# Performance work log

Hardware: AMD Instinct MI355X
Metric: run time of the kernel (lower is better)

## Reference

```python
import jax, jax.numpy as jnp
import numpy as np

B, C, H, W = 8, 128, 64, 64
NL = 3           # number of hidden variables (levels)
NC = C // 2      # channels per DAT block (q_c1 == kv_c1 == 64)
NH = 4           # heads
HC = NC // NH    # head channels = 16
KS = 4           # offset conv ksize == stride (pad=0 since ksize==stride)
EPS = 1e-5


def _norm_grid(ys, xs, Hk, Wk):
    g = jnp.stack(jnp.meshgrid(ys, xs, indexing='ij'), axis=-1)  # [Hk,Wk,2] (y,x)
    g = g.at[..., 0].set(g[..., 0] / (Hk - 1.0) * 2.0 - 1.0)
    g = g.at[..., 1].set(g[..., 1] / (Wk - 1.0) * 2.0 - 1.0)
    return g


def ref_points(Hk, Wk):
    return _norm_grid(jnp.linspace(0.5, Hk - 0.5, Hk), jnp.linspace(0.5, Wk - 0.5, Wk), Hk, Wk)


def q_grid(Hq, Wq):
    return _norm_grid(jnp.arange(Hq, dtype=jnp.float32), jnp.arange(Wq, dtype=jnp.float32), Hq, Wq)


def grid_sample(img, grid):
    # torch F.grid_sample: bilinear, align_corners=True, padding_mode='zeros'
    # img [B,C,H,W]; grid [B,*spatial,2] with (x,y) in [-1,1]
    Bi, Ci, Hi, Wi = img.shape
    sp = grid.shape[1:-1]
    g = grid.reshape(Bi, -1, 2)
    x = (g[..., 0] + 1.0) * 0.5 * (Wi - 1)
    y = (g[..., 1] + 1.0) * 0.5 * (Hi - 1)
    x0 = jnp.floor(x)
    y0 = jnp.floor(y)
    wx = x - x0
    wy = y - y0

    def gather(yi, xi):
        valid = ((yi >= 0) & (yi <= Hi - 1) & (xi >= 0) & (xi <= Wi - 1)).astype(img.dtype)
        yc = jnp.clip(yi, 0, Hi - 1).astype(jnp.int32)
        xc = jnp.clip(xi, 0, Wi - 1).astype(jnp.int32)
        vals = jax.vmap(lambda im, yy, xx: im[:, yy, xx])(img, yc, xc)  # [B,C,N]
        return vals * valid[:, None, :]

    out = (gather(y0, x0) * ((1 - wy) * (1 - wx))[:, None]
           + gather(y0, x0 + 1) * ((1 - wy) * wx)[:, None]
           + gather(y0 + 1, x0) * (wy * (1 - wx))[:, None]
           + gather(y0 + 1, x0 + 1) * (wy * wx)[:, None])
    return out.reshape((Bi, Ci) + sp)


def conv1x1(x, w, b=None):
    y = jnp.einsum('oc,bchw->bohw', w, x)
    return y if b is None else y + b[None, :, None, None]


def dat_block(q_in, kv_in, p):
    # DAttentionBaseline: n_groups=1, offset_range_factor=-1, use_pe=True,
    # dwc_pe=False, no_off=False, fixed_pe=False, log_cpb=False
    (pq_w, pq_b, dw_w, dw_b, ln_g, ln_b, pw_w,
     pk_w, pk_b, pv_w, pv_b, po_w, po_b, rpe) = p
    Bq, Cq, Hq, Wq = q_in.shape
    q = conv1x1(q_in, pq_w, pq_b)                              # [B,NC,H,W]
    # offset head: depthwise conv k4 s4 pad0 -> LayerNorm(channels) -> GELU -> 1x1 -> 2ch
    off = jax.lax.conv_general_dilated(
        q, dw_w, window_strides=(KS, KS), padding='VALID',
        dimension_numbers=('NCHW', 'OIHW', 'NCHW'),
        feature_group_count=NC) + dw_b[None, :, None, None]
    mu = off.mean(axis=1, keepdims=True)
    var = off.var(axis=1, keepdims=True)
    off = (off - mu) * jax.lax.rsqrt(var + EPS) * ln_g[None, :, None, None] + ln_b[None, :, None, None]
    off = jax.nn.gelu(off, approximate=False)
    offset = jnp.einsum('oc,bchw->bhwo', pw_w, off)            # [B,Hk,Wk,2] (y,x)
    Hk, Wk = offset.shape[1:3]
    Ns = Hk * Wk
    # offset_range_factor < 0 -> no tanh scaling, clamp(offset+ref, -1, 1)
    pos = jnp.clip(offset + ref_points(Hk, Wk)[None], -1.0, 1.0)
    xs = grid_sample(kv_in, pos[..., ::-1])                    # [B,Ckv,Hk,Wk]; grid as (x,y)
    xs = xs.reshape(Bq, kv_in.shape[1], Ns)
    k = jnp.einsum('oc,bcn->bon', pk_w, xs) + pk_b[None, :, None]
    v = jnp.einsum('oc,bcn->bon', pv_w, xs) + pv_b[None, :, None]
    qh = q.reshape(Bq, NH, HC, Hq * Wq)
    kh = k.reshape(Bq, NH, HC, Ns)
    vh = v.reshape(Bq, NH, HC, Ns)
    attn = jnp.einsum('bhcm,bhcn->bhmn', qh, kh) * (HC ** -0.5)
    # relative position bias: bilinear sample of rpe table at 0.5*(q_grid - pos)
    disp = (q_grid(Hq, Wq).reshape(1, Hq * Wq, 1, 2)
            - pos.reshape(Bq, 1, Ns, 2)) * 0.5                 # [B,HW,Ns,2] (y,x)
    bias = grid_sample(jnp.broadcast_to(rpe[None], (Bq,) + rpe.shape),
                       disp[..., ::-1])                        # [B,NH,HW,Ns]
    attn = jax.nn.softmax(attn + bias, axis=-1)
    out = jnp.einsum('bhmn,bhcn->bhcm', attn, vh).reshape(Bq, NC, Hq, Wq)
    return conv1x1(out, po_w, po_b)


def setup_inputs():
    key = jax.random.key(0)
    ks = jax.random.split(key, 16)
    s = 0.1
    NB = NL * (NL - 1) // 2
    return {
        'x0': jax.random.normal(ks[0], (B, C, H, W), jnp.float32),
        'x1': jax.random.normal(ks[1], (B, C, H, W), jnp.float32),
        'x2': jax.random.normal(ks[2], (B, C, H, W), jnp.float32),
        'pq_w': jax.random.normal(ks[3], (NB, NC, NC), jnp.float32) * s,
        'pq_b': jax.random.normal(ks[4], (NB, NC), jnp.float32) * s,
        'dw_w': jax.random.normal(ks[5], (NB, NC, 1, KS, KS), jnp.float32) * s,
        'dw_b': jax.random.normal(ks[6], (NB, NC), jnp.float32) * s,
        'ln_g': jnp.ones((NB, NC), jnp.float32),
        'ln_b': jnp.zeros((NB, NC), jnp.float32),
        'pw_w': jax.random.normal(ks[7], (NB, 2, NC), jnp.float32) * s,
        'pk_w': jax.random.normal(ks[8], (NB, NC, NC), jnp.float32) * s,
        'pk_b': jax.random.normal(ks[9], (NB, NC), jnp.float32) * s,
        'pv_w': jax.random.normal(ks[10], (NB, NC, NC), jnp.float32) * s,
        'pv_b': jax.random.normal(ks[11], (NB, NC), jnp.float32) * s,
        'po_w': jax.random.normal(ks[12], (NB, NC, NC), jnp.float32) * s,
        'po_b': jax.random.normal(ks[13], (NB, NC), jnp.float32) * s,
        'rpe': jax.random.normal(ks[14], (NB, NH, 2 * H - 1, 2 * W - 1), jnp.float32) * s,
    }


def reference(x0, x1, x2, pq_w, pq_b, dw_w, dw_b, ln_g, ln_b, pw_w,
              pk_w, pk_b, pv_w, pv_b, po_w, po_b, rpe):
    hidden = [x0, x1, x2]
    results = []
    num = 0
    for i in range(NL):
        res = hidden[i]
        for j in range(i):
            p = (pq_w[num], pq_b[num], dw_w[num], dw_b[num], ln_g[num], ln_b[num],
                 pw_w[num], pk_w[num], pk_b[num], pv_w[num], pv_b[num],
                 po_w[num], po_b[num], rpe[num])
            # rev=False, use_all_channels=False: q = hidden[i][:, :C//2], kv = hidden[j][:, :C//2]
            attn = dat_block(hidden[i][:, :NC], hidden[j][:, :NC], p)
            # res -= -attn with attn placed in the LAST q_c1 channels (zeros cat on first q_c2)
            res = jnp.concatenate([res[:, :C - NC], res[:, C - NC:] + attn], axis=1)
            num += 1
        results.append(res)
    return jnp.stack(results)  # [NL,B,C,H,W]
```

## Files before the change

### kernel.cpp

```cpp
#include <hip/hip_runtime.h>
#include <math.h>


typedef _Float16 f16x4 __attribute__((ext_vector_type(4)));
typedef float f32x4 __attribute__((ext_vector_type(4)));

__global__ __launch_bounds__(256) void k_copy(
    const float* __restrict__ x0, const float* __restrict__ x1,
    const float* __restrict__ x2, float* __restrict__ out) {
  int i = blockIdx.x * 256 + threadIdx.x;
  int lvl = i >> 20;
  int idx = i & 1048575;
  const float4* src = (lvl == 0) ? (const float4*)x0
                    : (lvl == 1) ? (const float4*)x1 : (const float4*)x2;
  ((float4*)out)[i] = src[idx];
}

__global__ __launch_bounds__(256) void k_qconv(
    const float* __restrict__ x1, const float* __restrict__ x2,
    const float* __restrict__ pq_w, const float* __restrict__ pq_b,
    float* __restrict__ q_buf) {
  int wg = blockIdx.x;
  int tile = wg & 15;
  int b = (wg >> 4) & 7;
  int og = (wg >> 7) & 7;
  int num = wg >> 10;
  const float* xin = (num == 0) ? x1 : x2;
  int px = tile * 256 + threadIdx.x;
  const float* xbase = xin + b * 524288 + px;
  const float* w = pq_w + num * 4096 + og * 512;
  float acc[8];
#pragma unroll
  for (int o = 0; o < 8; ++o) acc[o] = 0.f;
#pragma unroll 8
  for (int c = 0; c < 64; ++c) {
    float xv = xbase[c * 4096];
#pragma unroll
    for (int o = 0; o < 8; ++o) acc[o] += w[o * 64 + c] * xv;
  }
  float* qb = q_buf + ((num * 8 + b) * 64 + og * 8) * 4096 + px;
  const float* bias = pq_b + num * 64 + og * 8;
#pragma unroll
  for (int o = 0; o < 8; ++o) qb[o * 4096] = acc[o] + bias[o];
}

__global__ __launch_bounds__(256) void k_offset(
    const float* __restrict__ q_buf, const float* __restrict__ dw_w,
    const float* __restrict__ dw_b, const float* __restrict__ ln_g,
    const float* __restrict__ ln_b, const float* __restrict__ pw_w,
    float* __restrict__ pos_buf) {
  int wg = blockIdx.x;
  int num = wg >> 3;
  int n = threadIdx.x;
  int oy = n >> 4, ox = n & 15;
  const float* qb = q_buf + wg * 64 * 4096;
  float off[64];
  float sum = 0.f, sumsq = 0.f;
#pragma unroll
  for (int c = 0; c < 64; ++c) {
    const float* wp = dw_w + (num * 64 + c) * 16;
    const float* qp = qb + c * 4096 + oy * 256 + ox * 4;
    float4 r0 = *(const float4*)(qp);
    float4 r1 = *(const float4*)(qp + 64);
    float4 r2 = *(const float4*)(qp + 128);
    float4 r3 = *(const float4*)(qp + 192);
    float s = dw_b[num * 64 + c];
    s += wp[0] * r0.x + wp[1] * r0.y + wp[2] * r0.z + wp[3] * r0.w;
    s += wp[4] * r1.x + wp[5] * r1.y + wp[6] * r1.z + wp[7] * r1.w;
    s += wp[8] * r2.x + wp[9] * r2.y + wp[10] * r2.z + wp[11] * r2.w;
    s += wp[12] * r3.x + wp[13] * r3.y + wp[14] * r3.z + wp[15] * r3.w;
    off[c] = s;
    sum += s;
    sumsq += s * s;
  }
  float mu = sum * 0.015625f;
  float var = sumsq * 0.015625f - mu * mu;
  float rstd = rsqrtf(var + 1e-5f);
  float offy = 0.f, offx = 0.f;
#pragma unroll
  for (int c = 0; c < 64; ++c) {
    float g = (off[c] - mu) * rstd * ln_g[num * 64 + c] + ln_b[num * 64 + c];
    g = 0.5f * g * (1.f + erff(g * 0.70710678118654752f));
    offy += pw_w[num * 128 + c] * g;
    offx += pw_w[num * 128 + 64 + c] * g;
  }
  float ref_y = (0.5f + (float)oy) * (2.f / 15.f) - 1.f;
  float ref_x = (0.5f + (float)ox) * (2.f / 15.f) - 1.f;
  float py = fminf(fmaxf(offy + ref_y, -1.f), 1.f);
  float px = fminf(fmaxf(offx + ref_x, -1.f), 1.f);
  pos_buf[(wg * 256 + n) * 2 + 0] = py;
  pos_buf[(wg * 256 + n) * 2 + 1] = px;
}

__global__ __launch_bounds__(256) void k_sample(
    const float* __restrict__ x0, const float* __restrict__ x1,
    const float* __restrict__ pos_buf, float* __restrict__ xs_buf) {
  int wg = blockIdx.x;
  int cg = wg & 7;
  int b = (wg >> 3) & 7;
  int num = wg >> 6;
  const float* xj = (num == 2) ? x1 : x0;
  int n = threadIdx.x;
  int nb = num * 8 + b;
  float py = pos_buf[(nb * 256 + n) * 2 + 0];
  float px = pos_buf[(nb * 256 + n) * 2 + 1];
  float fy = (py + 1.f) * 31.5f;
  float fx = (px + 1.f) * 31.5f;
  float y0f = floorf(fy), x0f = floorf(fx);
  float wy = fy - y0f, wx = fx - x0f;
  int y0 = (int)y0f, xi0 = (int)x0f;
  int y1 = min(y0 + 1, 63), xi1 = min(xi0 + 1, 63);
  float w00 = (1.f - wy) * (1.f - wx), w01 = (1.f - wy) * wx;
  float w10 = wy * (1.f - wx), w11 = wy * wx;
  const float* xb = xj + b * 524288;
#pragma unroll
  for (int cc = 0; cc < 8; ++cc) {
    int c = cg * 8 + cc;
    const float* p = xb + c * 4096;
    float v = w00 * p[y0 * 64 + xi0] + w01 * p[y0 * 64 + xi1] +
              w10 * p[y1 * 64 + xi0] + w11 * p[y1 * 64 + xi1];
    xs_buf[(nb * 64 + c) * 256 + n] = v;
  }
}

__global__ __launch_bounds__(256) void k_kv(
    const float* __restrict__ xs_buf, const float* __restrict__ pk_w,
    const float* __restrict__ pk_b, const float* __restrict__ pv_w,
    const float* __restrict__ pv_b, _Float16* __restrict__ k16,
    _Float16* __restrict__ v16) {
  int wg = blockIdx.x;
  int which = wg & 1;
  int rest = wg >> 1;
  int nb = rest % 24;
  int og = rest / 24;
  int num = nb >> 3;
  const float* w = (which ? pv_w : pk_w) + num * 4096 + og * 512;
  const float* bias = (which ? pv_b : pk_b) + num * 64 + og * 8;
  _Float16* ob = (which ? v16 : k16) + (nb * 64 + og * 8) * 256;
  const float* xsb = xs_buf + nb * 64 * 256;
  int n = threadIdx.x;
  float acc[8];
#pragma unroll
  for (int o = 0; o < 8; ++o) acc[o] = 0.f;
#pragma unroll 8
  for (int c = 0; c < 64; ++c) {
    float xv = xsb[c * 256 + n];
#pragma unroll
    for (int o = 0; o < 8; ++o) acc[o] += w[o * 64 + c] * xv;
  }
#pragma unroll
  for (int o = 0; o < 8; ++o) ob[o * 256 + n] = (_Float16)(acc[o] + bias[o]);
}

__global__ __launch_bounds__(128) void k_padrpe(
    const float* __restrict__ rpe, float* __restrict__ tpad) {
  int wg = blockIdx.x;
  int tbl = wg >> 7;
  int r = wg & 127;
  int c = threadIdx.x;
  int rs = min(r, 126), cs = min(c, 126);
  tpad[tbl * 16384 + r * 128 + c] = rpe[tbl * 16129 + rs * 127 + cs];
}

__global__ __launch_bounds__(256) void k_attn(
    float* __restrict__ q_buf, const _Float16* __restrict__ k16,
    const _Float16* __restrict__ v16, const float* __restrict__ pos_buf,
    const float* __restrict__ tpad) {
  int wg = blockIdx.x;
  int mblock = wg & 15;
  int h = (wg >> 4) & 3;
  int b = (wg >> 6) & 7;
  int num = wg >> 9;
  int nb = num * 8 + b;
  int tid = threadIdx.x;
  int lane = tid & 63;
  int wave = __builtin_amdgcn_readfirstlane(tid >> 6);
  int l15 = lane & 15;
  int quad = lane >> 4;

  __shared__ __align__(16) float s_T[68 * 128];
  __shared__ float4 s_wt[256];
  __shared__ int s_off[256];

  {
    const float4* Ts = (const float4*)(tpad + (num * 4 + h) * 16384 + mblock * 512);
    float4* Td = (float4*)s_T;
#pragma unroll
    for (int i = 0; i < 8; ++i) Td[tid + i * 256] = Ts[tid + i * 256];
    if (tid < 128) Td[tid + 2048] = Ts[tid + 2048];
  }

  {
    float py = pos_buf[(nb * 256 + tid) * 2 + 0];
    float px = pos_buf[(nb * 256 + tid) * 2 + 1];
    float by = 31.5f * (1.f - py);
    float bx = 31.5f * (1.f - px);
    float iyf = floorf(by), ixf = floorf(bx);
    float wy = by - iyf, wx = bx - ixf;
    float uy = 1.f - wy, ux = 1.f - wx;
    s_off[tid] = (int)iyf * 128 + (int)ixf;
    s_wt[tid] = make_float4(uy * ux, uy * wx, wy * ux, wy * wx);
  }
  __syncthreads();

  int hc = nb * 64 + h * 16;
  const _Float16* kb = k16 + hc * 256;
  const _Float16* vb = v16 + hc * 256;
  float* qb = q_buf + hc * 4096;
  const float* Trow = s_T + wave * 128 + l15;

  f16x4 qf[4];
  f32x4 O[4];
  float L[4];
#pragma unroll
  for (int mt = 0; mt < 4; ++mt) {
    int m = mblock * 256 + wave * 64 + mt * 16 + l15;
#pragma unroll
    for (int j = 0; j < 4; ++j)
      qf[mt][j] = (_Float16)qb[(quad * 4 + j) * 4096 + m];
    O[mt][0] = 0.f; O[mt][1] = 0.f; O[mt][2] = 0.f; O[mt][3] = 0.f;
    L[mt] = 0.f;
  }

#pragma unroll 2
  for (int t = 0; t < 16; ++t) {
    f16x4 kf;
#pragma unroll
    for (int j = 0; j < 4; ++j)
      kf[j] = kb[(quad * 4 + j) * 256 + t * 16 + l15];
    f16x4 vf = *(const f16x4*)(vb + l15 * 256 + t * 16 + quad * 4);

    f32x4 S[4];
#pragma unroll
    for (int mt = 0; mt < 4; ++mt) {
      f32x4 Z = {0.f, 0.f, 0.f, 0.f};
      S[mt] = __builtin_amdgcn_mfma_f32_16x16x16f16(kf, qf[mt], Z, 0, 0, 0);
    }

    f16x4 pf[4];
#pragma unroll
    for (int r = 0; r < 4; ++r) {
      int off = s_off[t * 16 + quad * 4 + r];
      float4 wt = s_wt[t * 16 + quad * 4 + r];
#pragma unroll
      for (int mt = 0; mt < 4; ++mt) {
        const float* p = Trow + mt * 16 + off;
        float bias = wt.x * p[0] + wt.y * p[1] + wt.z * p[128] + wt.w * p[129];
        float s = fmaf(S[mt][r], 0.25f, bias);
        float e = __expf(s);
        L[mt] += e;
        pf[mt][r] = (_Float16)e;
      }
    }
#pragma unroll
    for (int mt = 0; mt < 4; ++mt)
      O[mt] = __builtin_amdgcn_mfma_f32_16x16x16f16(vf, pf[mt], O[mt], 0, 0, 0);
  }

#pragma unroll
  for (int mt = 0; mt < 4; ++mt) {
    float Lm = L[mt];
    Lm += __shfl_xor(Lm, 16);
    Lm += __shfl_xor(Lm, 32);
    float rinv = 1.f / Lm;
    int m = mblock * 256 + wave * 64 + mt * 16 + l15;
#pragma unroll
    for (int r = 0; r < 4; ++r)
      qb[(quad * 4 + r) * 4096 + m] = O[mt][r] * rinv;
  }
}

__global__ __launch_bounds__(256) void k_po(
    const float* __restrict__ attn_buf, const float* __restrict__ po_w,
    const float* __restrict__ po_b, float* __restrict__ out) {
  int wg = blockIdx.x;
  int tile = wg & 15;
  int b = (wg >> 4) & 7;
  int og = (wg >> 7) & 7;
  int l = (wg >> 10) + 1;
  int px = tile * 256 + threadIdx.x;
  int nlo = (l == 1) ? 0 : 1;
  int nPasses = (l == 1) ? 1 : 2;

  float acc[8];
#pragma unroll
  for (int o = 0; o < 8; ++o) acc[o] = 0.f;

  for (int s = 0; s < nPasses; ++s) {
    int num = nlo + s;
    const float* abase = attn_buf + (num * 8 + b) * 64 * 4096 + px;
    const float* w = po_w + num * 4096 + og * 512;
#pragma unroll 8
    for (int c = 0; c < 64; ++c) {
      float xv = abase[c * 4096];
#pragma unroll
      for (int o = 0; o < 8; ++o) acc[o] += w[o * 64 + c] * xv;
    }
  }

  float* ob = out + ((l * 8 + b) * 128 + 64 + og * 8) * 4096 + px;
#pragma unroll
  for (int o = 0; o < 8; ++o) {
    float bias = po_b[nlo * 64 + og * 8 + o];
    if (l == 2) bias += po_b[128 + og * 8 + o];
    ob[o * 4096] += acc[o] + bias;
  }
}

extern "C" void kernel_launch(void* const* d_in, const int* in_sizes, int n_in,
                              void* d_out, int out_size, void* d_ws,
                              size_t ws_size, hipStream_t stream) {
  const float* x0 = (const float*)d_in[0];
  const float* x1 = (const float*)d_in[1];
  const float* x2 = (const float*)d_in[2];
  const float* pq_w = (const float*)d_in[3];
  const float* pq_b = (const float*)d_in[4];
  const float* dw_w = (const float*)d_in[5];
  const float* dw_b = (const float*)d_in[6];
  const float* ln_g = (const float*)d_in[7];
  const float* ln_b = (const float*)d_in[8];
  const float* pw_w = (const float*)d_in[9];
  const float* pk_w = (const float*)d_in[10];
  const float* pk_b = (const float*)d_in[11];
  const float* pv_w = (const float*)d_in[12];
  const float* pv_b = (const float*)d_in[13];
  const float* po_w = (const float*)d_in[14];
  const float* po_b = (const float*)d_in[15];
  const float* rpe = (const float*)d_in[16];
  float* out = (float*)d_out;
  float* ws = (float*)d_ws;

  float* q_buf = ws;
  float* pos_buf = q_buf + 6291456;
  float* xs_buf = pos_buf + 12288;
  float* k_buf = xs_buf + 393216;
  float* v_buf = k_buf + 393216;
  float* tpad = xs_buf;
  _Float16* k16 = (_Float16*)k_buf;
  _Float16* v16 = (_Float16*)v_buf;

  hipLaunchKernelGGL(k_copy, dim3(12288), dim3(256), 0, stream, x0, x1, x2, out);
  hipLaunchKernelGGL(k_qconv, dim3(3072), dim3(256), 0, stream, x1, x2, pq_w,
                     pq_b, q_buf);
  hipLaunchKernelGGL(k_offset, dim3(24), dim3(256), 0, stream, q_buf, dw_w,
                     dw_b, ln_g, ln_b, pw_w, pos_buf);
  hipLaunchKernelGGL(k_sample, dim3(192), dim3(256), 0, stream, x0, x1,
                     pos_buf, xs_buf);
  hipLaunchKernelGGL(k_kv, dim3(384), dim3(256), 0, stream, xs_buf, pk_w, pk_b,
                     pv_w, pv_b, k16, v16);
  hipLaunchKernelGGL(k_padrpe, dim3(1536), dim3(128), 0, stream, rpe, tpad);
  hipLaunchKernelGGL(k_attn, dim3(1536), dim3(256), 0, stream, q_buf, k16,
                     v16, pos_buf, tpad);
  hipLaunchKernelGGL(k_po, dim3(2048), dim3(256), 0, stream, q_buf, po_w, po_b,
                     out);
}
```

Measured before the change: 281.3 us.

## Parallelize offset and sample kernels; store RPE table as fp16 and use exp2

k_offset now splits each pixel's 64 channels across 4 thread groups and combines the partial LayerNorm and projection sums with wave shuffles, launching 96 blocks instead of 24. k_sample handles 4 channels per block instead of 8, doubling the grid. In k_attn the shared-memory relative-position table is stored as fp16, halving LDS footprint and traffic. The softmax folds log2(e) into the bilinear weights and the score scale so it can call the hardware exp2 directly. The fp16 bias table lowers precision of the position bias, and the extra shuffles add a little overhead to the offset kernel.

```diff
diff --git a/kernel.cpp b/kernel.cpp
--- a/kernel.cpp
+++ b/kernel.cpp
@@ -50,14 +50,21 @@
     const float* __restrict__ ln_b, const float* __restrict__ pw_w,
     float* __restrict__ pos_buf) {
   int wg = blockIdx.x;
-  int num = wg >> 3;
-  int n = threadIdx.x;
+  int ptile = wg & 3;
+  int nb = wg >> 2;
+  int num = nb >> 3;
+  int tid = threadIdx.x;
+  int pix_lo = tid & 15;
+  int cg = (tid >> 4) & 3;
+  int pix_hi = tid >> 6;
+  int n = ptile * 64 + pix_hi * 16 + pix_lo;
   int oy = n >> 4, ox = n & 15;
-  const float* qb = q_buf + wg * 64 * 4096;
-  float off[64];
+  const float* qb = q_buf + nb * 64 * 4096;
+  float off_r[16];
   float sum = 0.f, sumsq = 0.f;
 #pragma unroll
-  for (int c = 0; c < 64; ++c) {
+  for (int cc = 0; cc < 16; ++cc) {
+    int c = cg * 16 + cc;
     const float* wp = dw_w + (num * 64 + c) * 16;
     const float* qp = qb + c * 4096 + oy * 256 + ox * 4;
     float4 r0 = *(const float4*)(qp);
@@ -69,36 +76,43 @@
     s += wp[4] * r1.x + wp[5] * r1.y + wp[6] * r1.z + wp[7] * r1.w;
     s += wp[8] * r2.x + wp[9] * r2.y + wp[10] * r2.z + wp[11] * r2.w;
     s += wp[12] * r3.x + wp[13] * r3.y + wp[14] * r3.z + wp[15] * r3.w;
-    off[c] = s;
+    off_r[cc] = s;
     sum += s;
     sumsq += s * s;
   }
+  sum += __shfl_xor(sum, 16);   sum += __shfl_xor(sum, 32);
+  sumsq += __shfl_xor(sumsq, 16); sumsq += __shfl_xor(sumsq, 32);
   float mu = sum * 0.015625f;
   float var = sumsq * 0.015625f - mu * mu;
   float rstd = rsqrtf(var + 1e-5f);
   float offy = 0.f, offx = 0.f;
 #pragma unroll
-  for (int c = 0; c < 64; ++c) {
-    float g = (off[c] - mu) * rstd * ln_g[num * 64 + c] + ln_b[num * 64 + c];
+  for (int cc = 0; cc < 16; ++cc) {
+    int c = cg * 16 + cc;
+    float g = (off_r[cc] - mu) * rstd * ln_g[num * 64 + c] + ln_b[num * 64 + c];
     g = 0.5f * g * (1.f + erff(g * 0.70710678118654752f));
     offy += pw_w[num * 128 + c] * g;
     offx += pw_w[num * 128 + 64 + c] * g;
   }
-  float ref_y = (0.5f + (float)oy) * (2.f / 15.f) - 1.f;
-  float ref_x = (0.5f + (float)ox) * (2.f / 15.f) - 1.f;
-  float py = fminf(fmaxf(offy + ref_y, -1.f), 1.f);
-  float px = fminf(fmaxf(offx + ref_x, -1.f), 1.f);
-  pos_buf[(wg * 256 + n) * 2 + 0] = py;
-  pos_buf[(wg * 256 + n) * 2 + 1] = px;
+  offy += __shfl_xor(offy, 16); offy += __shfl_xor(offy, 32);
+  offx += __shfl_xor(offx, 16); offx += __shfl_xor(offx, 32);
+  if (cg == 0) {
+    float ref_y = (0.5f + (float)oy) * (2.f / 15.f) - 1.f;
+    float ref_x = (0.5f + (float)ox) * (2.f / 15.f) - 1.f;
+    float py = fminf(fmaxf(offy + ref_y, -1.f), 1.f);
+    float px = fminf(fmaxf(offx + ref_x, -1.f), 1.f);
+    pos_buf[(nb * 256 + n) * 2 + 0] = py;
+    pos_buf[(nb * 256 + n) * 2 + 1] = px;
+  }
 }
 
 __global__ __launch_bounds__(256) void k_sample(
     const float* __restrict__ x0, const float* __restrict__ x1,
     const float* __restrict__ pos_buf, float* __restrict__ xs_buf) {
   int wg = blockIdx.x;
-  int cg = wg & 7;
-  int b = (wg >> 3) & 7;
-  int num = wg >> 6;
+  int cg = wg & 15;
+  int b = (wg >> 4) & 7;
+  int num = wg >> 7;
   const float* xj = (num == 2) ? x1 : x0;
   int n = threadIdx.x;
   int nb = num * 8 + b;
@@ -114,8 +128,8 @@
   float w10 = wy * (1.f - wx), w11 = wy * wx;
   const float* xb = xj + b * 524288;
 #pragma unroll
-  for (int cc = 0; cc < 8; ++cc) {
-    int c = cg * 8 + cc;
+  for (int cc = 0; cc < 4; ++cc) {
+    int c = cg * 4 + cc;
     const float* p = xb + c * 4096;
     float v = w00 * p[y0 * 64 + xi0] + w01 * p[y0 * 64 + xi1] +
               w10 * p[y1 * 64 + xi0] + w11 * p[y1 * 64 + xi1];
@@ -178,16 +192,28 @@
   int l15 = lane & 15;
   int quad = lane >> 4;
 
-  __shared__ __align__(16) float s_T[68 * 128];
+  __shared__ __align__(16) _Float16 s_T[68 * 128];
   __shared__ float4 s_wt[256];
   __shared__ int s_off[256];
 
   {
     const float4* Ts = (const float4*)(tpad + (num * 4 + h) * 16384 + mblock * 512);
-    float4* Td = (float4*)s_T;
-#pragma unroll
-    for (int i = 0; i < 8; ++i) Td[tid + i * 256] = Ts[tid + i * 256];
-    if (tid < 128) Td[tid + 2048] = Ts[tid + 2048];
+    f16x4* Td = (f16x4*)s_T;
+#pragma unroll
+    for (int i = 0; i < 8; ++i) {
+      float4 v = Ts[tid + i * 256];
+      f16x4 hv;
+      hv[0] = (_Float16)v.x; hv[1] = (_Float16)v.y;
+      hv[2] = (_Float16)v.z; hv[3] = (_Float16)v.w;
+      Td[tid + i * 256] = hv;
+    }
+    if (tid < 128) {
+      float4 v = Ts[tid + 2048];
+      f16x4 hv;
+      hv[0] = (_Float16)v.x; hv[1] = (_Float16)v.y;
+      hv[2] = (_Float16)v.z; hv[3] = (_Float16)v.w;
+      Td[tid + 2048] = hv;
+    }
   }
 
   {
@@ -198,8 +224,10 @@
     float iyf = floorf(by), ixf = floorf(bx);
     float wy = by - iyf, wx = bx - ixf;
     float uy = 1.f - wy, ux = 1.f - wx;
+    const float L2E = 1.44269504088896341f;
     s_off[tid] = (int)iyf * 128 + (int)ixf;
-    s_wt[tid] = make_float4(uy * ux, uy * wx, wy * ux, wy * wx);
+    s_wt[tid] = make_float4(uy * ux * L2E, uy * wx * L2E,
+                            wy * ux * L2E, wy * wx * L2E);
   }
   __syncthreads();
 
@@ -207,7 +235,7 @@
   const _Float16* kb = k16 + hc * 256;
   const _Float16* vb = v16 + hc * 256;
   float* qb = q_buf + hc * 4096;
-  const float* Trow = s_T + wave * 128 + l15;
+  const _Float16* Trow = s_T + wave * 128 + l15;
 
   f16x4 qf[4];
   f32x4 O[4];
@@ -244,10 +272,11 @@
       float4 wt = s_wt[t * 16 + quad * 4 + r];
 #pragma unroll
       for (int mt = 0; mt < 4; ++mt) {
-        const float* p = Trow + mt * 16 + off;
-        float bias = wt.x * p[0] + wt.y * p[1] + wt.z * p[128] + wt.w * p[129];
-        float s = fmaf(S[mt][r], 0.25f, bias);
-        float e = __expf(s);
+        const _Float16* p = Trow + mt * 16 + off;
+        float bias = wt.x * (float)p[0] + wt.y * (float)p[1] +
+                     wt.z * (float)p[128] + wt.w * (float)p[129];
+        float s = fmaf(S[mt][r], 0.36067376022224085f, bias);
+        float e = __builtin_amdgcn_exp2f(s);
         L[mt] += e;
         pf[mt][r] = (_Float16)e;
       }
@@ -342,9 +371,9 @@
   hipLaunchKernelGGL(k_copy, dim3(12288), dim3(256), 0, stream, x0, x1, x2, out);
   hipLaunchKernelGGL(k_qconv, dim3(3072), dim3(256), 0, stream, x1, x2, pq_w,
                      pq_b, q_buf);
-  hipLaunchKernelGGL(k_offset, dim3(24), dim3(256), 0, stream, q_buf, dw_w,
+  hipLaunchKernelGGL(k_offset, dim3(96), dim3(256), 0, stream, q_buf, dw_w,
                      dw_b, ln_g, ln_b, pw_w, pos_buf);
-  hipLaunchKernelGGL(k_sample, dim3(192), dim3(256), 0, stream, x0, x1,
+  hipLaunchKernelGGL(k_sample, dim3(384), dim3(256), 0, stream, x0, x1,
                      pos_buf, xs_buf);
   hipLaunchKernelGGL(k_kv, dim3(384), dim3(256), 0, stream, xs_buf, pk_w, pk_b,
                      pv_w, pv_b, k16, v16);
```

Result: slower. 540.9 us (+92.3%).
